# Kernel tuning notes

Measured on AMD Instinct MI355X. Metric: run time of the kernel, lower is better.

## Reference

```python
import jax, jax.numpy as jnp
import numpy as np

B, T, O, H = 64, 1000, 61, 256
IN0, IN1 = 320, 2 * H  # layer0 input = 8*40 flattened feats; layer1 input = bidirectional concat


def setup_inputs() -> dict:
    key = jax.random.key(0)
    ks = jax.random.split(key, 12)
    rn = lambda k, shape: (jax.random.normal(k, shape, dtype=jnp.float32) * 0.05)
    inp = {}
    inp["batch"] = jax.random.normal(ks[0], (B, T, 8, 40), dtype=jnp.float32)
    lengths = np.random.RandomState(0).randint(T // 2, T + 1, size=B).astype(np.int64)
    inp["lengths"] = jnp.asarray(lengths)
    # GRU params stacked over directions: [2, 3H, in], [2, 3H, H], biases [2, 3H]
    inp["w_ih_l0"] = rn(ks[1], (2, 3 * H, IN0))
    inp["w_hh_l0"] = rn(ks[2], (2, 3 * H, H))
    inp["b_ih_l0"] = rn(ks[3], (2, 3 * H))
    inp["b_hh_l0"] = rn(ks[4], (2, 3 * H))
    inp["w_ih_l1"] = rn(ks[5], (2, 3 * H, IN1))
    inp["w_hh_l1"] = rn(ks[6], (2, 3 * H, H))
    inp["b_ih_l1"] = rn(ks[7], (2, 3 * H))
    inp["b_hh_l1"] = rn(ks[8], (2, 3 * H))
    inp["fc_w"] = rn(ks[9], (O, 2 * H))
    inp["fc_b"] = rn(ks[10], (O,))
    return inp


def _gru_dir(x, w_ih, w_hh, b_ih, b_hh, reverse):
    # x: [T, B, in] -> ys: [T, B, H]; torch GRU cell semantics
    def step(h, xt):
        gi = xt @ w_ih.T + b_ih          # [B, 3H]
        gh = h @ w_hh.T + b_hh           # [B, 3H]
        i_r, i_z, i_n = jnp.split(gi, 3, axis=-1)
        h_r, h_z, h_n = jnp.split(gh, 3, axis=-1)
        r = jax.nn.sigmoid(i_r + h_r)
        z = jax.nn.sigmoid(i_z + h_z)
        n = jnp.tanh(i_n + r * h_n)
        h_new = (1.0 - z) * n + z * h
        return h_new, h_new
    h0 = jnp.zeros((x.shape[1], w_hh.shape[-1]), x.dtype)
    _, ys = jax.lax.scan(step, h0, x, reverse=reverse)
    return ys


def _bigru_layer(x, w_ih, w_hh, b_ih, b_hh):
    fwd = _gru_dir(x, w_ih[0], w_hh[0], b_ih[0], b_hh[0], reverse=False)
    bwd = _gru_dir(x, w_ih[1], w_hh[1], b_ih[1], b_hh[1], reverse=True)
    return jnp.concatenate([fwd, bwd], axis=-1)  # [T, B, 2H]


def reference(batch, lengths, w_ih_l0, w_hh_l0, b_ih_l0, b_hh_l0,
              w_ih_l1, w_hh_l1, b_ih_l1, b_hh_l1, fc_w, fc_b):
    b, t = batch.shape[0], batch.shape[1]
    x = jnp.swapaxes(batch, 2, 3).reshape(b, t, -1)   # transpose(2,3).flatten(2) -> [B,T,320]
    x = jnp.swapaxes(x, 0, 1)                          # [T, B, 320] (time-major like torch GRU)
    h1 = _bigru_layer(x, w_ih_l0, w_hh_l0, b_ih_l0, b_hh_l0)
    h2 = _bigru_layer(h1, w_ih_l1, w_hh_l1, b_ih_l1, b_hh_l1)
    out = h2 @ fc_w.T + fc_b                           # [T, B, O]
    out = jnp.swapaxes(out, 0, 1)                      # [B, T, O]
    # gather first lengths[i] timesteps of each sample, concatenated
    L = np.asarray(lengths)
    mask = np.arange(t)[None, :] < L[:, None]
    bi, ti = np.nonzero(mask)
    return out[bi, ti]                                 # [sum(lengths), O]
```

## Files before the change

### kernel.cpp

```cpp
#include <hip/hip_runtime.h>
#include <cstdint>
#include <cstddef>


typedef __attribute__((ext_vector_type(8))) __bf16 bf16x8;
typedef __attribute__((ext_vector_type(4))) float f32x4;
typedef __attribute__((ext_vector_type(4))) unsigned int u32x4;

#define AS1 __attribute__((address_space(1)))
#define AS3 __attribute__((address_space(3)))

#define LOG2E 1.44269504089f
#define SRZ  (-1.44269504089f)
#define SN   (2.88539008177f)

__device__ __forceinline__ void async_ld16(const void* g, void* l) {
  __builtin_amdgcn_global_load_lds((const AS1 unsigned int*)g,
                                   (AS3 unsigned int*)l, 16, 0, 0);
}

__device__ __forceinline__ f32x4 mfma16(u32x4 a, u32x4 b, f32x4 c) {
  return __builtin_amdgcn_mfma_f32_16x16x32_bf16(
      __builtin_bit_cast(bf16x8, a), __builtin_bit_cast(bf16x8, b), c, 0, 0, 0);
}

__device__ __forceinline__ unsigned short f2b(float f) {
  unsigned int u = __float_as_uint(f);
  u += 0x7fffu + ((u >> 16) & 1u);
  return (unsigned short)(u >> 16);
}
__device__ __forceinline__ float b2f(unsigned short s) {
  return __uint_as_float(((unsigned int)s) << 16);
}
__device__ __forceinline__ unsigned int cvtpk(float lo, float hi) {
  unsigned int r;
  asm("v_cvt_pk_bf16_f32 %0, %1, %2" : "=v"(r) : "v"(lo), "v"(hi));
  return r;
}
__device__ __forceinline__ float lo16(unsigned int d) {
  return __uint_as_float(d << 16);
}
__device__ __forceinline__ float hi16(unsigned int d) {
  return __uint_as_float(d & 0xffff0000u);
}
__device__ __forceinline__ float gload(const float* p, size_t i) { return p[i]; }
__device__ __forceinline__ float gload(const unsigned short* p, size_t i) { return b2f(p[i]); }

__device__ __forceinline__ float sigm2(float xs) {
  return __builtin_amdgcn_rcpf(1.0f + __builtin_amdgcn_exp2f(xs));
}
__device__ __forceinline__ float tanh2(float ys) {
  return __builtin_fmaf(-2.0f,
      __builtin_amdgcn_rcpf(1.0f + __builtin_amdgcn_exp2f(ys)), 1.0f);
}

__device__ __forceinline__ void lds_barrier() {
  asm volatile("" ::: "memory");
  __builtin_amdgcn_s_waitcnt(0xC07F);
  __builtin_amdgcn_s_barrier();
  asm volatile("" ::: "memory");
}

__global__ void cast_bf16_kernel(const float* __restrict__ src,
                                 unsigned short* __restrict__ dst, int n) {
  const int i = blockIdx.x * 256 + threadIdx.x;
  if (i < n) dst[i] = f2b(src[i]);
}

__global__ void cast_w_kernel(const float* __restrict__ src,
                              unsigned short* __restrict__ dst, int n,
                              int in_dim) {
  const int i = blockIdx.x * 256 + threadIdx.x;
  if (i < n) {
    const int row = (i / in_dim) % 768;
    const float s = (row < 512) ? SRZ : SN;
    dst[i] = f2b(s * src[i]);
  }
}

__global__ void bias_fuse_kernel(const float* __restrict__ bih,
                                 const float* __restrict__ bhh,
                                 float* __restrict__ fb) {
  const int n = blockIdx.x * 256 + threadIdx.x;
  if (n < 1536) {
    const int dir = n >> 9 >> 1 ? 1 : (n / 768);
    const int rr = n - dir * 768;
    const float s = (rr < 512) ? SRZ : SN;
    float v = bih[dir * 768 + rr];
    if (rr < 512) v += bhh[dir * 768 + rr];
    fb[n] = s * v;
  }
}

__global__ void transpose_x_kernel(const float* __restrict__ batch,
                                   unsigned short* __restrict__ xb) {
  const int t = blockIdx.x, b = blockIdx.y, i = threadIdx.x;
  const float v = batch[((size_t)b * 1000 + t) * 320 + (i & 7) * 40 + (i >> 3)];
  xb[((size_t)t * 64 + b) * 320 + i] = f2b(v);
}

template <typename CT, bool PERM>
__global__ __launch_bounds__(256) void gemm_bt_kernel(
    const unsigned short* __restrict__ A, const unsigned short* __restrict__ W,
    const float* __restrict__ bias, CT* __restrict__ C, int M, int N, int K) {
  __shared__ __align__(16) unsigned short As[4096];
  __shared__ __align__(16) unsigned short Bs[4096];
  const int tid = threadIdx.x;
  const int lane = tid & 63;
  const int wv = tid >> 6;
  const int mBase = blockIdx.x * 128;
  const int nBase = blockIdx.y * 128;

  const int s0 = tid, s1 = tid + 256;
  const int r0 = ((s0 >> 6) << 4) | (s0 & 15), c0 = ((s0 >> 4) & 3) * 8;
  const int r1 = ((s1 >> 6) << 4) | (s1 & 15), c1 = ((s1 >> 4) & 3) * 8;

  const unsigned short* Arow0 = A + (size_t)(mBase + r0) * K + c0;
  const unsigned short* Arow1 = A + (size_t)(mBase + r1) * K + c1;
  const unsigned short* Wrow0 = W + (size_t)(nBase + r0) * K + c0;
  const unsigned short* Wrow1 = W + (size_t)(nBase + r1) * K + c1;

  char* lA = (char*)As;
  char* lB = (char*)Bs;
  char* dstA0 = lA + wv * 1024;
  char* dstA1 = lA + 4096 + wv * 1024;
  char* dstB0 = lB + wv * 1024;
  char* dstB1 = lB + 4096 + wv * 1024;

  f32x4 acc[4][4] = {};
  const int mh = (wv >> 1) * 64, nh = (wv & 1) * 64;
  const u32x4* As4 = (const u32x4*)As;
  const u32x4* Bs4 = (const u32x4*)Bs;

  for (int k0 = 0; k0 < K; k0 += 32) {
    __syncthreads();
    async_ld16(Arow0 + k0, dstA0);
    async_ld16(Arow1 + k0, dstA1);
    async_ld16(Wrow0 + k0, dstB0);
    async_ld16(Wrow1 + k0, dstB1);
    __syncthreads();
    u32x4 a[4], b[4];
#pragma unroll
    for (int mt = 0; mt < 4; ++mt) a[mt] = As4[((mh >> 4) + mt) * 64 + lane];
#pragma unroll
    for (int nt = 0; nt < 4; ++nt) b[nt] = Bs4[((nh >> 4) + nt) * 64 + lane];
#pragma unroll
    for (int mt = 0; mt < 4; ++mt)
#pragma unroll
      for (int nt = 0; nt < 4; ++nt)
        acc[mt][nt] = mfma16(a[mt], b[nt], acc[mt][nt]);
  }

  if constexpr (PERM) {
    const int t = (mBase + mh) >> 6;
#pragma unroll
    for (int p = 0; p < 2; ++p) {
      const int nb0 = nBase + nh + p * 32;
      const int dir = (nb0 >= 768) ? 1 : 0;
      const int np = nb0 - dir * 768;
      const int g = np >> 8;
      const int ww = (np >> 5) & 7;
      const float bn0 = bias[nb0 + (lane & 15)];
      const float bn1 = bias[nb0 + 16 + (lane & 15)];
#pragma unroll
      for (int mt = 0; mt < 4; ++mt) {
        const size_t slot = (size_t)t * 64 + (size_t)(mt * 2 + dir) * 8 + ww;
        if constexpr (sizeof(CT) == 2) {
          u32x4 v;
          v[0] = cvtpk(acc[mt][2 * p][0] + bn0, acc[mt][2 * p][1] + bn0);
          v[1] = cvtpk(acc[mt][2 * p][2] + bn0, acc[mt][2 * p][3] + bn0);
          v[2] = cvtpk(acc[mt][2 * p + 1][0] + bn1, acc[mt][2 * p + 1][1] + bn1);
          v[3] = cvtpk(acc[mt][2 * p + 1][2] + bn1, acc[mt][2 * p + 1][3] + bn1);
          *(u32x4*)((unsigned short*)C + slot * 1536 + (size_t)g * 512 +
                    (size_t)lane * 8) = v;
        } else {
#pragma unroll
          for (int rs = 0; rs < 2; ++rs) {
            f32x4 v = {acc[mt][2 * p][2 * rs] + bn0,
                       acc[mt][2 * p][2 * rs + 1] + bn0,
                       acc[mt][2 * p + 1][2 * rs] + bn1,
                       acc[mt][2 * p + 1][2 * rs + 1] + bn1};
            *(f32x4*)((float*)C + slot * 1536 + (size_t)(g * 2 + rs) * 256 +
                      (size_t)lane * 4) = v;
          }
        }
      }
    }
  } else {
#pragma unroll
    for (int nt = 0; nt < 4; ++nt) {
      const int n = nBase + nh + nt * 16 + (lane & 15);
      const float bn = bias[n];
#pragma unroll
      for (int mt = 0; mt < 4; ++mt) {
        const int mrow = mBase + mh + mt * 16 + ((lane >> 4) << 2);
#pragma unroll
        for (int r = 0; r < 4; ++r) {
          const float v = acc[mt][nt][r] + bn;
          if constexpr (sizeof(CT) == 2)
            ((unsigned short*)C)[(size_t)(mrow + r) * N + n] = f2b(v);
          else
            ((float*)C)[(size_t)(mrow + r) * N + n] = v;
        }
      }
    }
  }
}

#define GBLOCK(G)                                                              \
  {                                                                            \
    _Pragma("unroll") for (int kt = 0; kt < 6; ++kt) {                         \
      acc[0][G] = mfma16(a[kt], wv[0][G][kt], acc[0][G]);                      \
      acc[1][G] = mfma16(a[kt], wv[1][G][kt], acc[1][G]);                      \
    }                                                                          \
    _Pragma("unroll") for (int kk = 0; kk < 2; ++kk) {                         \
      u32x4 bf0 = *(const u32x4*)(wlds +                                       \
          (((w * 12 + (0 * 3 + (G)) * 2 + kk) << 10) + lane * 16));            \
      u32x4 bf1 = *(const u32x4*)(wlds +                                       \
          (((w * 12 + (1 * 3 + (G)) * 2 + kk) << 10) + lane * 16));            \
      acc[0][G] = mfma16(a[6 + kk], bf0, acc[0][G]);                           \
      acc[1][G] = mfma16(a[6 + kk], bf1, acc[1][G]);                           \
    }                                                                          \
  }

template <typename GT>
__global__ __launch_bounds__(512, 2) void gru_fast_kernel(
    const GT* __restrict__ gi,
    const unsigned short* __restrict__ whh,
    const float* __restrict__ bhh,
    unsigned short* __restrict__ hout) {
  constexpr int E = (int)sizeof(GT);
  constexpr int CH = (E * 1536) / 1024;
  constexpr bool DB = (E == 2);
  constexpr int HB = DB ? 18432 : 9216;
  extern __shared__ __align__(16) char smem[];
  char* wlds = smem;
  char* hl   = smem + 98304;
  char* glds = smem + 98304 + HB;
  const int tid = threadIdx.x;
  const int lane = tid & 63;
  const int w = tid >> 6;
  const int c = lane & 15;
  const int q = lane >> 4;
  const int dir = blockIdx.x & 1;
  const int sb = (blockIdx.x >> 1) * 16;

  for (int i = tid; i < HB / 2; i += 512) ((unsigned short*)hl)[i] = 0;

  const int u0 = 32 * w + c;
  const float bhn0 = SN * bhh[dir * 768 + 512 + u0];
  const float bhn1 = SN * bhh[dir * 768 + 512 + u0 + 16];

  const unsigned short* wb =
      whh + (size_t)dir * 196608 + (size_t)u0 * 256 + q * 8;
  u32x4 wv[2][3][6];
#pragma unroll
  for (int j = 0; j < 2; ++j)
#pragma unroll
    for (int g = 0; g < 3; ++g) {
      const unsigned short* p = wb + (size_t)(g * 256 + 16 * j) * 256;
#pragma unroll
      for (int kt = 0; kt < 6; ++kt) wv[j][g][kt] = *(const u32x4*)(p + kt * 32);
#pragma unroll
      for (int kk = 0; kk < 2; ++kk) {
        u32x4 tmp = *(const u32x4*)(p + (6 + kk) * 32);
        *(u32x4*)(wlds + (((w * 12 + (j * 3 + g) * 2 + kk) << 10) + lane * 16)) = tmp;
      }
    }
#pragma unroll
  for (int j = 0; j < 2; ++j)
#pragma unroll
    for (int g = 0; g < 3; ++g)
#pragma unroll
      for (int kt = 0; kt < 6; ++kt)
        asm volatile("" : "+v"(wv[j][g][kt]));

  float h0[4] = {0.f, 0.f, 0.f, 0.f}, h1[4] = {0.f, 0.f, 0.f, 0.f};

  const int t0 = dir ? 999 : 0;
  unsigned short* hp = hout + ((size_t)t0 * 64 + sb) * 512 + dir * 256 + u0;
  const ptrdiff_t gstep = (dir ? -1 : 1) * (ptrdiff_t)(64 * 1536);
  const ptrdiff_t hstep = (dir ? -1 : 1) * (ptrdiff_t)(64 * 512);

  char* gdw = glds + w * (1536 * E);
  const size_t slot0 =
      (size_t)t0 * 64 + (size_t)((blockIdx.x >> 1) * 2 + dir) * 8 + w;
  const GT* gp2 = gi + slot0 * 1536 + (size_t)lane * (16 / E);
#pragma unroll
  for (int i = 0; i < CH; ++i)
    async_ld16(gp2 + i * (1024 / E), gdw + i * 1024);
  gp2 += gstep;

  __syncthreads();

  const char* habase = hl + c * 576 + q * 16;
  const int hw0 = q * 4 * 288 + u0;

  auto body = [&](int rd, int wr) {
    u32x4 a[8];
#pragma unroll
    for (int kt = 0; kt < 8; ++kt)
      a[kt] = *(const u32x4*)(habase + rd + kt * 64);
    if constexpr (!DB) lds_barrier();

    f32x4 acc[2][3] = {};
    GBLOCK(0)

    asm volatile("s_waitcnt vmcnt(0)" ::: "memory");
    u32x4 raw[CH];
#pragma unroll
    for (int i = 0; i < CH; ++i)
      raw[i] = *(const u32x4*)(gdw + i * 1024 + lane * 16);

    float pvA[3][4], pvB[3][4];
    if constexpr (E == 2) {
#pragma unroll
      for (int g = 0; g < 3; ++g)
#pragma unroll
        for (int r = 0; r < 4; ++r) {
          const unsigned int d0 = raw[g][r >> 1];
          const unsigned int d1 = raw[g][2 + (r >> 1)];
          pvA[g][r] = (r & 1) ? hi16(d0) : lo16(d0);
          pvB[g][r] = (r & 1) ? hi16(d1) : lo16(d1);
        }
    } else {
#pragma unroll
      for (int g = 0; g < 3; ++g)
#pragma unroll
        for (int r = 0; r < 4; ++r) {
          const f32x4 f = __builtin_bit_cast(f32x4, raw[g * 2 + (r >> 1)]);
          pvA[g][r] = f[r & 1];
          pvB[g][r] = f[2 + (r & 1)];
        }
    }

    float rr0[4], rr1[4];
#pragma unroll
    for (int r = 0; r < 4; ++r) {
      rr0[r] = sigm2(pvA[0][r] + acc[0][0][r]);
      rr1[r] = sigm2(pvB[0][r] + acc[1][0][r]);
    }

    GBLOCK(2)

    float nn0[4], nn1[4];
#pragma unroll
    for (int r = 0; r < 4; ++r) {
      nn0[r] = tanh2(__builtin_fmaf(rr0[r], acc[0][2][r] + bhn0, pvA[2][r]));
      nn1[r] = tanh2(__builtin_fmaf(rr1[r], acc[1][2][r] + bhn1, pvB[2][r]));
    }

    GBLOCK(1)

    asm volatile("s_waitcnt lgkmcnt(0)" ::: "memory");
#pragma unroll
    for (int i = 0; i < CH; ++i)
      async_ld16(gp2 + i * (1024 / E), gdw + i * 1024);
    gp2 += gstep;

    unsigned short* hls = (unsigned short*)(hl + wr);
#pragma unroll
    for (int r = 0; r < 4; ++r) {
      const float zz0 = sigm2(pvA[1][r] + acc[0][1][r]);
      const float hv0 = __builtin_fmaf(zz0, h0[r] - nn0[r], nn0[r]);
      h0[r] = hv0;
      const float zz1 = sigm2(pvB[1][r] + acc[1][1][r]);
      const float hv1 = __builtin_fmaf(zz1, h1[r] - nn1[r], nn1[r]);
      h1[r] = hv1;
      const unsigned int pk = cvtpk(hv0, hv1);
      const unsigned int pkh = pk >> 16;
      hls[hw0 + r * 288] = (unsigned short)pk;
      hls[hw0 + r * 288 + 16] = (unsigned short)pkh;
      hp[(size_t)(q * 4 + r) * 512] = (unsigned short)pk;
      hp[(size_t)(q * 4 + r) * 512 + 16] = (unsigned short)pkh;
    }
    hp += hstep;
    lds_barrier();
  };

  if constexpr (DB) {
    for (int it = 0; it < 500; ++it) {
      body(0, 9216);
      body(9216, 0);
    }
  } else {
    for (int step = 0; step < 1000; ++step) body(0, 0);
  }
  asm volatile("s_waitcnt vmcnt(0)" ::: "memory");
}

template <typename GT>
__global__ __launch_bounds__(1024) void gru_layer_kernel(
    const GT* __restrict__ gi, const unsigned short* __restrict__ whh,
    const float* __restrict__ bhh, unsigned short* __restrict__ hout) {
  __shared__ __align__(16) unsigned short hbf[16][264];
  __shared__ __align__(16) float gh[16][780];
  const int tid = threadIdx.x;
  const int lane = tid & 63;
  const int wv = tid >> 6;
  const int dir = blockIdx.x & 1;
  const int sb = (blockIdx.x >> 1) * 16;
  const int j = tid & 255;
  const int si = tid >> 8;

  float hreg[4] = {0.f, 0.f, 0.f, 0.f};
#pragma unroll
  for (int i = 0; i < 4; ++i) hbf[si + i * 4][j] = 0;

  const float bh_n = SN * bhh[dir * 768 + 512 + j];

  const unsigned short* wl = whh + (size_t)dir * 768 * 256 +
                             (size_t)(wv * 48 + (lane & 15)) * 256 +
                             ((lane >> 4) * 8);
  const char* habase = (const char*)hbf + (lane & 15) * 528 + ((lane >> 4) << 4);
  const int srow = (lane >> 4) * 4;

  __syncthreads();

  for (int step = 0; step < 1000; ++step) {
    const int t = dir ? (999 - step) : step;
    float p_ir[4], p_iz[4], p_in[4];
#pragma unroll
    for (int i = 0; i < 4; ++i) {
      const int s = si + i * 4;
      const size_t gib = ((size_t)t * 64 + (sb + s)) * 1536 + dir * 768 + j;
      p_ir[i] = gload(gi, gib);
      p_iz[i] = gload(gi, gib + 256);
      p_in[i] = gload(gi, gib + 512);
    }
    u32x4 a[8];
#pragma unroll
    for (int kt = 0; kt < 8; ++kt) a[kt] = *(const u32x4*)(habase + kt * 64);
#pragma unroll
    for (int ntd = 0; ntd < 3; ++ntd) {
      f32x4 acc = {0.f, 0.f, 0.f, 0.f};
#pragma unroll
      for (int kt = 0; kt < 8; ++kt) {
        u32x4 bfrag = *(const u32x4*)(wl + ntd * (16 * 256) + kt * 32);
        acc = mfma16(a[kt], bfrag, acc);
      }
      const int gcol = (wv * 3 + ntd) * 16 + (lane & 15);
#pragma unroll
      for (int r = 0; r < 4; ++r) gh[srow + r][gcol] = acc[r];
    }
    __syncthreads();
#pragma unroll
    for (int i = 0; i < 4; ++i) {
      const int s = si + i * 4;
      const float r = sigm2(p_ir[i] + gh[s][j]);
      const float z = sigm2(p_iz[i] + gh[s][256 + j]);
      const float n = tanh2(__builtin_fmaf(r, gh[s][512 + j] + bh_n, p_in[i]));
      const float h = __builtin_fmaf(z, hreg[i] - n, n);
      hreg[i] = h;
      const unsigned short hb = f2b(h);
      hbf[s][j] = hb;
      hout[((size_t)t * 64 + (sb + s)) * 512 + dir * 256 + j] = hb;
    }
    __syncthreads();
  }
}

__global__ void prefix_kernel(const int* __restrict__ raw,
                              int* __restrict__ pref, int* __restrict__ lens) {
  if (threadIdx.x == 0) {
    const int stride = (raw[1] == 0 && raw[3] == 0 && raw[5] == 0) ? 2 : 1;
    int a = 0;
    for (int b = 0; b < 64; ++b) {
      const int L = raw[b * stride];
      pref[b] = a;
      lens[b] = L;
      a += L;
    }
  }
}

__global__ __launch_bounds__(256) void fc_kernel(
    const unsigned short* __restrict__ h2, const unsigned short* __restrict__ fcw,
    const float* __restrict__ fcb, const int* __restrict__ lens,
    const int* __restrict__ pref, float* __restrict__ out) {
  __shared__ __align__(16) unsigned short hrow[4][512];
  const int b = blockIdx.y;
  const int sub = threadIdx.x >> 6, lane = threadIdx.x & 63;
  const int t = blockIdx.x * 4 + sub;
  *(u32x4*)&hrow[sub][lane * 8] =
      *(const u32x4*)&h2[((size_t)t * 64 + b) * 512 + lane * 8];
  __syncthreads();
  const int len = lens[b];
  if (lane < 61 && t < len) {
    float acc = fcb[lane];
    const unsigned short* wr = fcw + (size_t)lane * 512;
#pragma unroll 4
    for (int k = 0; k < 512; k += 8) {
      u32x4 w4 = *(const u32x4*)(wr + k);
      u32x4 h4 = *(const u32x4*)(&hrow[sub][k]);
#pragma unroll
      for (int qq = 0; qq < 4; ++qq) {
        acc += __uint_as_float(w4[qq] << 16) * __uint_as_float(h4[qq] << 16);
        acc += __uint_as_float(w4[qq] & 0xffff0000u) * __uint_as_float(h4[qq] & 0xffff0000u);
      }
    }
    out[((size_t)pref[b] + t) * 61 + lane] = acc;
  }
}

template <typename GT>
static void run_pipeline(const float* batch, const int* lengths_raw,
                         const float* w_ih_l0, const float* w_hh_l0,
                         const float* b_ih_l0, const float* b_hh_l0,
                         const float* w_ih_l1, const float* w_hh_l1,
                         const float* b_ih_l1, const float* b_hh_l1,
                         const float* fc_w, const float* fc_b, float* out,
                         char* ws, hipStream_t stream) {
  size_t off = 0;
  auto alloc = [&](size_t bytes) -> char* {
    char* p = ws + off;
    off += (bytes + 255) & ~(size_t)255;
    return p;
  };
  char* pool = alloc((size_t)64000 * 512 * 2);
  unsigned short* xb = (unsigned short*)pool;
  unsigned short* h1 = (unsigned short*)pool;
  unsigned short* h2 = (unsigned short*)pool;
  GT*             gi   = (GT*)alloc((size_t)64064 * 1536 * sizeof(GT));
  unsigned short* wih0 = (unsigned short*)alloc((size_t)1536 * 320 * 2);
  unsigned short* wih1 = (unsigned short*)alloc((size_t)1536 * 512 * 2);
  unsigned short* whh0 = (unsigned short*)alloc((size_t)1536 * 256 * 2);
  unsigned short* whh1 = (unsigned short*)alloc((size_t)1536 * 256 * 2);
  unsigned short* fcwb = (unsigned short*)alloc((size_t)61 * 512 * 2);
  float*          fb0  = (float*)alloc(1536 * 4);
  float*          fb1  = (float*)alloc(1536 * 4);
  int*            pref = (int*)alloc(256);
  int*            lens = (int*)alloc(256);

  auto castw = [&](const float* s, unsigned short* d, int n, int in_dim) {
    cast_w_kernel<<<dim3((n + 255) / 256), dim3(256), 0, stream>>>(s, d, n, in_dim);
  };
  castw(w_ih_l0, wih0, 2 * 768 * 320, 320);
  castw(w_hh_l0, whh0, 2 * 768 * 256, 256);
  castw(w_ih_l1, wih1, 2 * 768 * 512, 512);
  castw(w_hh_l1, whh1, 2 * 768 * 256, 256);
  cast_bf16_kernel<<<dim3((61 * 512 + 255) / 256), dim3(256), 0, stream>>>(
      fc_w, fcwb, 61 * 512);
  bias_fuse_kernel<<<dim3(6), dim3(256), 0, stream>>>(b_ih_l0, b_hh_l0, fb0);
  bias_fuse_kernel<<<dim3(6), dim3(256), 0, stream>>>(b_ih_l1, b_hh_l1, fb1);

  transpose_x_kernel<<<dim3(1000, 64), dim3(320), 0, stream>>>(batch, xb);

  const int HB = (sizeof(GT) == 2) ? 18432 : 9216;
  const int GRU_LDS = 98304 + HB + 8 * 1536 * (int)sizeof(GT);
  const bool big_lds =
      hipFuncSetAttribute(reinterpret_cast<const void*>(gru_fast_kernel<GT>),
                          hipFuncAttributeMaxDynamicSharedMemorySize,
                          GRU_LDS) == hipSuccess;

  auto gemm = [&](const unsigned short* A, const unsigned short* W,
                  const float* fb, GT* Cc, int M, int N, int K) {
    if (big_lds)
      gemm_bt_kernel<GT, true><<<dim3(500, 12), dim3(256), 0, stream>>>(
          A, W, fb, Cc, M, N, K);
    else
      gemm_bt_kernel<GT, false><<<dim3(500, 12), dim3(256), 0, stream>>>(
          A, W, fb, Cc, M, N, K);
  };
  auto gru = [&](GT* g, unsigned short* w, const float* b, unsigned short* h) {
    if (big_lds)
      gru_fast_kernel<GT><<<dim3(8), dim3(512), GRU_LDS, stream>>>(g, w, b, h);
    else
      gru_layer_kernel<GT><<<dim3(8), dim3(1024), 0, stream>>>(g, w, b, h);
  };

  gemm(xb, wih0, fb0, gi, 64000, 1536, 320);
  gru(gi, whh0, b_hh_l0, h1);
  gemm(h1, wih1, fb1, gi, 64000, 1536, 512);
  gru(gi, whh1, b_hh_l1, h2);

  prefix_kernel<<<dim3(1), dim3(64), 0, stream>>>(lengths_raw, pref, lens);
  fc_kernel<<<dim3(250, 64), dim3(256), 0, stream>>>(h2, fcwb, fc_b, lens, pref, out);
}

extern "C" void kernel_launch(void* const* d_in, const int* in_sizes, int n_in,
                              void* d_out, int out_size, void* d_ws, size_t ws_size,
                              hipStream_t stream) {
  (void)in_sizes; (void)n_in; (void)out_size;
  const float* batch   = (const float*)d_in[0];
  const int*   lengths = (const int*)d_in[1];
  const float* w_ih_l0 = (const float*)d_in[2];
  const float* w_hh_l0 = (const float*)d_in[3];
  const float* b_ih_l0 = (const float*)d_in[4];
  const float* b_hh_l0 = (const float*)d_in[5];
  const float* w_ih_l1 = (const float*)d_in[6];
  const float* w_hh_l1 = (const float*)d_in[7];
  const float* b_ih_l1 = (const float*)d_in[8];
  const float* b_hh_l1 = (const float*)d_in[9];
  const float* fc_w    = (const float*)d_in[10];
  const float* fc_b    = (const float*)d_in[11];
  float* out = (float*)d_out;
  char* ws = (char*)d_ws;

  const size_t NEED_FP32 = 470000000ull;
  if (ws_size >= NEED_FP32) {
    run_pipeline<float>(batch, lengths, w_ih_l0, w_hh_l0, b_ih_l0, b_hh_l0,
                        w_ih_l1, w_hh_l1, b_ih_l1, b_hh_l1, fc_w, fc_b, out,
                        ws, stream);
  } else {
    run_pipeline<unsigned short>(batch, lengths, w_ih_l0, w_hh_l0, b_ih_l0,
                                 b_hh_l0, w_ih_l1, w_hh_l1, b_ih_l1, b_hh_l1,
                                 fc_w, fc_b, out, ws, stream);
  }
}
```

Baseline: 3.707 ms.

## Split GRU recurrence across paired blocks with global-memory hidden-state exchange

```diff
diff --git a/kernel.cpp b/kernel.cpp
--- a/kernel.cpp
+++ b/kernel.cpp
@@ -90,6 +90,10 @@
     if (rr < 512) v += bhh[dir * 768 + rr];
     fb[n] = s * v;
   }
+}
+
+__global__ void clear_flags_kernel(unsigned int* __restrict__ f) {
+  f[threadIdx.x] = 0u;
 }
 
 __global__ void transpose_x_kernel(const float* __restrict__ batch,
@@ -224,30 +228,37 @@
   }
 
 template <typename GT>
-__global__ __launch_bounds__(512, 2) void gru_fast_kernel(
+__global__ __launch_bounds__(256, 1) void gru_split_kernel(
     const GT* __restrict__ gi,
     const unsigned short* __restrict__ whh,
     const float* __restrict__ bhh,
-    unsigned short* __restrict__ hout) {
+    unsigned short* __restrict__ hout,
+    unsigned int* __restrict__ flags,
+    char* __restrict__ exch) {
   constexpr int E = (int)sizeof(GT);
   constexpr int CH = (E * 1536) / 1024;
   constexpr bool DB = (E == 2);
   constexpr int HB = DB ? 18432 : 9216;
   extern __shared__ __align__(16) char smem[];
   char* wlds = smem;
-  char* hl   = smem + 98304;
-  char* glds = smem + 98304 + HB;
+  char* hl   = smem + 49152;
+  char* glds = smem + 49152 + HB;
   const int tid = threadIdx.x;
   const int lane = tid & 63;
   const int w = tid >> 6;
   const int c = lane & 15;
   const int q = lane >> 4;
-  const int dir = blockIdx.x & 1;
-  const int sb = (blockIdx.x >> 1) * 16;
-
-  for (int i = tid; i < HB / 2; i += 512) ((unsigned short*)hl)[i] = 0;
-
-  const int u0 = 32 * w + c;
+  const int bx = blockIdx.x;
+  const int dir = bx & 1;
+  const int sgrp = (bx >> 1) & 3;
+  const int half = bx >> 3;
+  const int pbx = bx ^ 8;
+  const int sb = sgrp * 16;
+  const int u0 = half * 128 + 32 * w + c;
+  const int pu0 = (1 - half) * 128 + 32 * w + c;
+
+  for (int i = tid; i < HB / 2; i += 256) ((unsigned short*)hl)[i] = 0;
+
   const float bhn0 = SN * bhh[dir * 768 + 512 + u0];
   const float bhn1 = SN * bhh[dir * 768 + 512 + u0 + 16];
 
@@ -284,7 +295,7 @@
 
   char* gdw = glds + w * (1536 * E);
   const size_t slot0 =
-      (size_t)t0 * 64 + (size_t)((blockIdx.x >> 1) * 2 + dir) * 8 + w;
+      (size_t)t0 * 64 + (size_t)((sgrp * 2 + dir) * 8 + half * 4 + w);
   const GT* gp2 = gi + slot0 * 1536 + (size_t)lane * (16 / E);
 #pragma unroll
   for (int i = 0; i < CH; ++i)
@@ -296,7 +307,13 @@
   const char* habase = hl + c * 576 + q * 16;
   const int hw0 = q * 4 * 288 + u0;
 
-  auto body = [&](int rd, int wr) {
+  const size_t exoff = ((size_t)bx * 256 + tid) * 16;
+  const size_t pxoff = ((size_t)pbx * 256 + tid) * 16;
+  unsigned int* fm = flags + (bx * 4 + w);
+  const unsigned int* fp = flags + (pbx * 4 + w);
+  int guard = 1 << 22;
+
+  auto body = [&](int rd, int wr, int step) {
     u32x4 a[8];
 #pragma unroll
     for (int kt = 0; kt < 8; ++kt)
@@ -352,13 +369,8 @@
 
     GBLOCK(1)
 
-    asm volatile("s_waitcnt lgkmcnt(0)" ::: "memory");
-#pragma unroll
-    for (int i = 0; i < CH; ++i)
-      async_ld16(gp2 + i * (1024 / E), gdw + i * 1024);
-    gp2 += gstep;
-
     unsigned short* hls = (unsigned short*)(hl + wr);
+    unsigned int pks[4];
 #pragma unroll
     for (int r = 0; r < 4; ++r) {
       const float zz0 = sigm2(pvA[1][r] + acc[0][1][r]);
@@ -368,23 +380,59 @@
       const float hv1 = __builtin_fmaf(zz1, h1[r] - nn1[r], nn1[r]);
       h1[r] = hv1;
       const unsigned int pk = cvtpk(hv0, hv1);
-      const unsigned int pkh = pk >> 16;
+      pks[r] = pk;
       hls[hw0 + r * 288] = (unsigned short)pk;
-      hls[hw0 + r * 288 + 16] = (unsigned short)pkh;
-      hp[(size_t)(q * 4 + r) * 512] = (unsigned short)pk;
-      hp[(size_t)(q * 4 + r) * 512 + 16] = (unsigned short)pkh;
-    }
+      hls[hw0 + r * 288 + 16] = (unsigned short)(pk >> 16);
+    }
+
+    char* exb = exch + ((step & 1) ? 65536 : 0);
+    u32x4 ex;
+    ex[0] = cvtpk(h0[0], h0[1]);
+    ex[1] = cvtpk(h0[2], h0[3]);
+    ex[2] = cvtpk(h1[0], h1[1]);
+    ex[3] = cvtpk(h1[2], h1[3]);
+    *(u32x4*)(exb + exoff) = ex;
+    asm volatile("s_waitcnt vmcnt(0)" ::: "memory");
+    if (lane == 0)
+      __hip_atomic_store(fm, (unsigned int)(step + 1), __ATOMIC_RELEASE,
+                         __HIP_MEMORY_SCOPE_AGENT);
+    while (__hip_atomic_load(fp, __ATOMIC_ACQUIRE, __HIP_MEMORY_SCOPE_AGENT) <=
+           (unsigned int)step) {
+      if (--guard < 0) break;
+    }
+    const u32x4 px = *(const u32x4*)(exb + pxoff);
+
+    asm volatile("s_waitcnt lgkmcnt(0)" ::: "memory");
+#pragma unroll
+    for (int i = 0; i < CH; ++i)
+      async_ld16(gp2 + i * (1024 / E), gdw + i * 1024);
+    gp2 += gstep;
+#pragma unroll
+    for (int r = 0; r < 4; ++r) {
+      hp[(size_t)(q * 4 + r) * 512] = (unsigned short)pks[r];
+      hp[(size_t)(q * 4 + r) * 512 + 16] = (unsigned short)(pks[r] >> 16);
+    }
+
+    hls[(q * 4 + 0) * 288 + pu0] = (unsigned short)px[0];
+    hls[(q * 4 + 1) * 288 + pu0] = (unsigned short)(px[0] >> 16);
+    hls[(q * 4 + 2) * 288 + pu0] = (unsigned short)px[1];
+    hls[(q * 4 + 3) * 288 + pu0] = (unsigned short)(px[1] >> 16);
+    hls[(q * 4 + 0) * 288 + pu0 + 16] = (unsigned short)px[2];
+    hls[(q * 4 + 1) * 288 + pu0 + 16] = (unsigned short)(px[2] >> 16);
+    hls[(q * 4 + 2) * 288 + pu0 + 16] = (unsigned short)px[3];
+    hls[(q * 4 + 3) * 288 + pu0 + 16] = (unsigned short)(px[3] >> 16);
+
     hp += hstep;
     lds_barrier();
   };
 
   if constexpr (DB) {
     for (int it = 0; it < 500; ++it) {
-      body(0, 9216);
-      body(9216, 0);
+      body(0, 9216, 2 * it);
+      body(9216, 0, 2 * it + 1);
     }
   } else {
-    for (int step = 0; step < 1000; ++step) body(0, 0);
+    for (int step = 0; step < 1000; ++step) body(0, 0, step);
   }
   asm volatile("s_waitcnt vmcnt(0)" ::: "memory");
 }
@@ -529,6 +577,8 @@
   unsigned short* fcwb = (unsigned short*)alloc((size_t)61 * 512 * 2);
   float*          fb0  = (float*)alloc(1536 * 4);
   float*          fb1  = (float*)alloc(1536 * 4);
+  unsigned int*   flags = (unsigned int*)alloc(256);
+  char*           exch  = alloc(131072);
   int*            pref = (int*)alloc(256);
   int*            lens = (int*)alloc(256);
 
@@ -546,10 +596,9 @@
 
   transpose_x_kernel<<<dim3(1000, 64), dim3(320), 0, stream>>>(batch, xb);
 
-  const int HB = (sizeof(GT) == 2) ? 18432 : 9216;
-  const int GRU_LDS = 98304 + HB + 8 * 1536 * (int)sizeof(GT);
+  const int GRU_LDS = 86016;
   const bool big_lds =
-      hipFuncSetAttribute(reinterpret_cast<const void*>(gru_fast_kernel<GT>),
+      hipFuncSetAttribute(reinterpret_cast<const void*>(gru_split_kernel<GT>),
                           hipFuncAttributeMaxDynamicSharedMemorySize,
                           GRU_LDS) == hipSuccess;
 
@@ -563,10 +612,13 @@
           A, W, fb, Cc, M, N, K);
   };
   auto gru = [&](GT* g, unsigned short* w, const float* b, unsigned short* h) {
-    if (big_lds)
-      gru_fast_kernel<GT><<<dim3(8), dim3(512), GRU_LDS, stream>>>(g, w, b, h);
-    else
+    if (big_lds) {
+      clear_flags_kernel<<<dim3(1), dim3(64), 0, stream>>>(flags);
+      gru_split_kernel<GT><<<dim3(16), dim3(256), GRU_LDS, stream>>>(
+          g, w, b, h, flags, exch);
+    } else {
       gru_layer_kernel<GT><<<dim3(8), dim3(1024), 0, stream>>>(g, w, b, h);
+    }
   };
 
   gemm(xb, wih0, fb0, gi, 64000, 1536, 320);
```

After: 8.876 ms. 2.39x slower.

## Permute hidden-state layout for packed 32-bit stores and relax vmcnt wait

Applied to the files above, without the earlier changes.

```diff
diff --git a/kernel.cpp b/kernel.cpp
--- a/kernel.cpp
+++ b/kernel.cpp
@@ -75,6 +75,22 @@
     const int row = (i / in_dim) % 768;
     const float s = (row < 512) ? SRZ : SN;
     dst[i] = f2b(s * src[i]);
+  }
+}
+
+__global__ void cast_w_perm_kernel(const float* __restrict__ src,
+                                   unsigned short* __restrict__ dst, int n,
+                                   int in_dim, int scaled) {
+  const int i = blockIdx.x * 256 + threadIdx.x;
+  if (i < n) {
+    const int row = i / in_dim;
+    const int p = i - row * in_dim;
+    const int hi = p >> 8, pr = p & 255;
+    const int w = pr >> 5, c2 = pr & 31;
+    const int k = hi * 256 + w * 32 + (c2 & 1) * 16 + (c2 >> 1);
+    float s = 1.0f;
+    if (scaled) s = ((row % 768) < 512) ? SRZ : SN;
+    dst[i] = f2b(s * src[(size_t)row * in_dim + k]);
   }
 }
 
@@ -278,9 +294,10 @@
   float h0[4] = {0.f, 0.f, 0.f, 0.f}, h1[4] = {0.f, 0.f, 0.f, 0.f};
 
   const int t0 = dir ? 999 : 0;
-  unsigned short* hp = hout + ((size_t)t0 * 64 + sb) * 512 + dir * 256 + u0;
+  unsigned int* hp = (unsigned int*)hout +
+                     ((size_t)t0 * 64 + sb) * 256 + dir * 128 + w * 16 + c;
   const ptrdiff_t gstep = (dir ? -1 : 1) * (ptrdiff_t)(64 * 1536);
-  const ptrdiff_t hstep = (dir ? -1 : 1) * (ptrdiff_t)(64 * 512);
+  const ptrdiff_t hstep = (dir ? -1 : 1) * (ptrdiff_t)(64 * 256);
 
   char* gdw = glds + w * (1536 * E);
   const size_t slot0 =
@@ -294,9 +311,9 @@
   __syncthreads();
 
   const char* habase = hl + c * 576 + q * 16;
-  const int hw0 = q * 4 * 288 + u0;
-
-  auto body = [&](int rd, int wr) {
+  const int hwb = q * 4 * 576 + w * 64 + c * 4;
+
+  auto body = [&](int rd, int wr, bool first) {
     u32x4 a[8];
 #pragma unroll
     for (int kt = 0; kt < 8; ++kt)
@@ -306,7 +323,8 @@
     f32x4 acc[2][3] = {};
     GBLOCK(0)
 
-    asm volatile("s_waitcnt vmcnt(0)" ::: "memory");
+    if (first) asm volatile("s_waitcnt vmcnt(0)" ::: "memory");
+    else       asm volatile("s_waitcnt vmcnt(4)" ::: "memory");
     u32x4 raw[CH];
 #pragma unroll
     for (int i = 0; i < CH; ++i)
@@ -368,23 +386,23 @@
       const float hv1 = __builtin_fmaf(zz1, h1[r] - nn1[r], nn1[r]);
       h1[r] = hv1;
       const unsigned int pk = cvtpk(hv0, hv1);
-      const unsigned int pkh = pk >> 16;
-      hls[hw0 + r * 288] = (unsigned short)pk;
-      hls[hw0 + r * 288 + 16] = (unsigned short)pkh;
-      hp[(size_t)(q * 4 + r) * 512] = (unsigned short)pk;
-      hp[(size_t)(q * 4 + r) * 512 + 16] = (unsigned short)pkh;
+      *(unsigned int*)((char*)hls + hwb + r * 576) = pk;
+      hp[(size_t)(q * 4 + r) * 256] = pk;
     }
     hp += hstep;
     lds_barrier();
   };
 
   if constexpr (DB) {
-    for (int it = 0; it < 500; ++it) {
-      body(0, 9216);
-      body(9216, 0);
+    body(0, 9216, true);
+    body(9216, 0, false);
+    for (int it = 1; it < 500; ++it) {
+      body(0, 9216, false);
+      body(9216, 0, false);
     }
   } else {
-    for (int step = 0; step < 1000; ++step) body(0, 0);
+    body(0, 0, true);
+    for (int step = 1; step < 1000; ++step) body(0, 0, false);
   }
   asm volatile("s_waitcnt vmcnt(0)" ::: "memory");
 }
@@ -532,26 +550,39 @@
   int*            pref = (int*)alloc(256);
   int*            lens = (int*)alloc(256);
 
-  auto castw = [&](const float* s, unsigned short* d, int n, int in_dim) {
-    cast_w_kernel<<<dim3((n + 255) / 256), dim3(256), 0, stream>>>(s, d, n, in_dim);
-  };
-  castw(w_ih_l0, wih0, 2 * 768 * 320, 320);
-  castw(w_hh_l0, whh0, 2 * 768 * 256, 256);
-  castw(w_ih_l1, wih1, 2 * 768 * 512, 512);
-  castw(w_hh_l1, whh1, 2 * 768 * 256, 256);
-  cast_bf16_kernel<<<dim3((61 * 512 + 255) / 256), dim3(256), 0, stream>>>(
-      fc_w, fcwb, 61 * 512);
-  bias_fuse_kernel<<<dim3(6), dim3(256), 0, stream>>>(b_ih_l0, b_hh_l0, fb0);
-  bias_fuse_kernel<<<dim3(6), dim3(256), 0, stream>>>(b_ih_l1, b_hh_l1, fb1);
-
-  transpose_x_kernel<<<dim3(1000, 64), dim3(320), 0, stream>>>(batch, xb);
-
   const int HB = (sizeof(GT) == 2) ? 18432 : 9216;
   const int GRU_LDS = 98304 + HB + 8 * 1536 * (int)sizeof(GT);
   const bool big_lds =
       hipFuncSetAttribute(reinterpret_cast<const void*>(gru_fast_kernel<GT>),
                           hipFuncAttributeMaxDynamicSharedMemorySize,
                           GRU_LDS) == hipSuccess;
+
+  auto castw_lin = [&](const float* s, unsigned short* d, int n, int in_dim) {
+    cast_w_kernel<<<dim3((n + 255) / 256), dim3(256), 0, stream>>>(s, d, n, in_dim);
+  };
+  auto castw_perm = [&](const float* s, unsigned short* d, int n, int in_dim,
+                        int scaled) {
+    cast_w_perm_kernel<<<dim3((n + 255) / 256), dim3(256), 0, stream>>>(
+        s, d, n, in_dim, scaled);
+  };
+
+  castw_lin(w_ih_l0, wih0, 2 * 768 * 320, 320);
+  if (big_lds) {
+    castw_perm(w_hh_l0, whh0, 2 * 768 * 256, 256, 1);
+    castw_perm(w_hh_l1, whh1, 2 * 768 * 256, 256, 1);
+    castw_perm(w_ih_l1, wih1, 2 * 768 * 512, 512, 1);
+    castw_perm(fc_w, fcwb, 61 * 512, 512, 0);
+  } else {
+    castw_lin(w_hh_l0, whh0, 2 * 768 * 256, 256);
+    castw_lin(w_hh_l1, whh1, 2 * 768 * 256, 256);
+    castw_lin(w_ih_l1, wih1, 2 * 768 * 512, 512);
+    cast_bf16_kernel<<<dim3((61 * 512 + 255) / 256), dim3(256), 0, stream>>>(
+        fc_w, fcwb, 61 * 512);
+  }
+  bias_fuse_kernel<<<dim3(6), dim3(256), 0, stream>>>(b_ih_l0, b_hh_l0, fb0);
+  bias_fuse_kernel<<<dim3(6), dim3(256), 0, stream>>>(b_ih_l1, b_hh_l1, fb1);
+
+  transpose_x_kernel<<<dim3(1000, 64), dim3(320), 0, stream>>>(batch, xb);
 
   auto gemm = [&](const unsigned short* A, const unsigned short* W,
                   const float* fb, GT* Cc, int M, int N, int K) {
```

After: 3.637 ms, median of 2. Within noise of the previous version (-1.9%).
